# Kernel tuning notes

Measured on AMD Instinct MI355X. Metric: run time of the kernel, lower is better.

The kernel has to match this reference:

```python
import jax, jax.numpy as jnp
import numpy as np

N_TOK = 2048      # flattened batch*seq tokens
D_MODEL = 1024    # in_features
D_INT = 512       # d_intermediate
N_EXPERTS = 8     # n_routed_experts
TOP_K = 2         # n_activated_experts


def setup_inputs() -> dict:
    key = jax.random.key(0)
    k1, k2, k3, k4, k5 = jax.random.split(key, 5)
    x = jax.random.normal(k1, (N_TOK, D_MODEL), dtype=jnp.float32)
    indices = jax.random.randint(k2, (N_TOK, TOP_K), 0, N_EXPERTS, dtype=jnp.int32)
    # router combine weights (normalized over top-k like a softmax router)
    weights = jax.nn.softmax(jax.random.normal(k3, (N_TOK, TOP_K), dtype=jnp.float32), axis=-1)
    # tokens-per-expert counts, consistent with indices (as the router would supply)
    counts = jnp.bincount(indices.reshape(-1), length=N_EXPERTS).astype(jnp.int32)
    # expert weights: fc1 -> 2*d_int (gated MLP), fc2 -> d_model; kaiming-ish scale
    s1 = 1.0 / np.sqrt(D_MODEL)
    s2 = 1.0 / np.sqrt(D_INT)
    fc1_weight = jax.random.uniform(k4, (N_EXPERTS, 2 * D_INT, D_MODEL), jnp.float32, -s1, s1)
    fc2_weight = jax.random.uniform(k5, (N_EXPERTS, D_MODEL, D_INT), jnp.float32, -s2, s2)
    return {"x": x, "weights": weights, "indices": indices, "counts": counts,
            "fc1_weight": fc1_weight, "fc2_weight": fc2_weight}


def reference(x, weights, indices, counts, fc1_weight, fc2_weight):
    # Dense dispatch-free formulation: run every token through every expert's
    # gated MLP, then gather the per-slot expert output. Identical math to the
    # sort / grouped-GEMM / scatter path for the selected (token, expert) pairs.
    # h: (n_tok, n_experts, 2*d_int)
    h = jnp.einsum('td,egd->teg', x, fc1_weight)
    y, z = jnp.split(h, 2, axis=-1)
    a = y * jax.nn.silu(z)  # GatedMLP: y * activation(z)
    # expert outputs: (n_tok, n_experts, d_model)
    out = jnp.einsum('tei,edi->ted', a, fc2_weight)
    # gather the chosen expert output for each of the top-k slots: (n_tok, k, d_model)
    per_slot = jnp.take_along_axis(out, indices[:, :, None], axis=1)
    # combine: z = bmm(weights[:, None], x_by_expert).squeeze(1)
    return jnp.einsum('tk,tkd->td', weights, per_slot)
```

## Files before the change

### kernel.cpp

```cpp
#include <hip/hip_runtime.h>

typedef unsigned short u16;
typedef unsigned int u32;
using short8  = __attribute__((ext_vector_type(8))) short;
using floatx4 = __attribute__((ext_vector_type(4))) float;

#define N_TOK   2048
#define D_MODEL 1024
#define D_INT   512
#define NE      8
#define NPAIR   (N_TOK * 2)
#define ROWS_PAD 5120

#define O_META   0
#define O_ROWOF  4096
#define O_XG     65536
#define O_ACT    10551296
#define O_O2     15794176
#define O_FC1B   36765696
#define O_FC2B   53542912

static __device__ inline u16 f2bf(float f) {
    u32 u = __builtin_bit_cast(u32, f);
    u = (u + 0x7fffu + ((u >> 16) & 1u)) >> 16;
    return (u16)u;
}
static __device__ inline u32 pack2(float a, float b) {
    return (u32)f2bf(a) | ((u32)f2bf(b) << 16);
}

__global__ __launch_bounds__(256) void route_kernel(const int* __restrict__ indices,
                                                    const int* __restrict__ counts,
                                                    int* __restrict__ meta,
                                                    int* __restrict__ row_of) {
    __shared__ int cnt[256][NE];
    __shared__ int off[NE];
    int t = threadIdx.x;
    int idx[16];
    #pragma unroll
    for (int i = 0; i < 16; i++) idx[i] = indices[t * 16 + i];
    int loc[NE];
    #pragma unroll
    for (int e = 0; e < NE; e++) {
        int c = 0;
        #pragma unroll
        for (int i = 0; i < 16; i++) c += (idx[i] == e);
        loc[e] = c;
        cnt[t][e] = c;
    }
    if (t == 0) {
        int acc = 0;
        #pragma unroll
        for (int e = 0; e < NE; e++) {
            off[e] = acc;
            meta[e] = acc;
            acc += ((counts[e] + 127) >> 7) << 7;
        }
        meta[8] = acc;
    }
    __syncthreads();
    for (int d = 1; d < 256; d <<= 1) {
        int v[NE];
        #pragma unroll
        for (int e = 0; e < NE; e++) v[e] = (t >= d) ? cnt[t - d][e] : 0;
        __syncthreads();
        #pragma unroll
        for (int e = 0; e < NE; e++) cnt[t][e] += v[e];
        __syncthreads();
    }
    #pragma unroll
    for (int e = 0; e < NE; e++) cnt[t][e] -= loc[e];
    __syncthreads();
    #pragma unroll
    for (int i = 0; i < 16; i++) {
        int e = idx[i];
        int r = cnt[t][e]++;
        row_of[t * 16 + i] = off[e] + r;
    }
}

__global__ __launch_bounds__(128) void gather_kernel(const float* __restrict__ x,
                                                     const int* __restrict__ row_of,
                                                     u16* __restrict__ Xg) {
    int t = blockIdx.x;
    int tid = threadIdx.x;
    int r0 = row_of[2 * t], r1 = row_of[2 * t + 1];
    const floatx4* src = reinterpret_cast<const floatx4*>(x + (size_t)t * D_MODEL);
    floatx4 a = src[tid * 2];
    floatx4 b = src[tid * 2 + 1];
    uint4 o;
    o.x = pack2(a[0], a[1]); o.y = pack2(a[2], a[3]);
    o.z = pack2(b[0], b[1]); o.w = pack2(b[2], b[3]);
    *reinterpret_cast<uint4*>(Xg + (size_t)r0 * D_MODEL + tid * 8) = o;
    *reinterpret_cast<uint4*>(Xg + (size_t)r1 * D_MODEL + tid * 8) = o;
}

__global__ void convert_w(const float* __restrict__ fc1, const float* __restrict__ fc2,
                          u16* __restrict__ fc1b, u16* __restrict__ fc2b) {
    size_t v = (size_t)blockIdx.x * 256 + threadIdx.x;
    const float* src; u16* dst; size_t off;
    if (v < 1048576) { src = fc1; dst = fc1b; off = v * 8; }
    else             { src = fc2; dst = fc2b; off = (v - 1048576) * 8; }
    const floatx4* s4 = reinterpret_cast<const floatx4*>(src + off);
    floatx4 a = s4[0], b = s4[1];
    uint4 o;
    o.x = pack2(a[0], a[1]); o.y = pack2(a[2], a[3]);
    o.z = pack2(b[0], b[1]); o.w = pack2(b[2], b[3]);
    *reinterpret_cast<uint4*>(dst + off) = o;
}

__global__ __launch_bounds__(256) void gemm1_kernel(
    const u16* __restrict__ Xg, const u16* __restrict__ fc1b,
    u16* __restrict__ Act, const int* __restrict__ meta) {
    __shared__ u16 As[4096];
    __shared__ u16 Bs[4096];
    __shared__ int soff[9];
    int tid = threadIdx.x;
    if (tid < 9) soff[tid] = meta[tid];
    __syncthreads();
    int row0 = blockIdx.y * 128;
    if (row0 >= soff[8]) return;
    int e = 0;
    while (soff[e + 1] <= row0) e++;
    int bx = blockIdx.x;
    const u16* A  = Xg + (size_t)row0 * 1024;
    const u16* Be = fc1b + (size_t)e * 1024 * 1024;

    int lane = tid & 63, w = tid >> 6;
    int m0 = (w >> 1) * 64, n0 = (w & 1) * 32;
    int lr = lane & 15, kq = lane >> 4;

    floatx4 acc[4][4];
    #pragma unroll
    for (int i = 0; i < 4; i++)
        #pragma unroll
        for (int j = 0; j < 4; j++) acc[i][j] = (floatx4){0.f, 0.f, 0.f, 0.f};

    for (int k0 = 0; k0 < 1024; k0 += 32) {
        #pragma unroll
        for (int s = 0; s < 2; s++) {
            int v = tid + s * 256;
            int row = v >> 2, kb = v & 3;
            *reinterpret_cast<uint4*>(&As[(kb * 128 + row) * 8]) =
                *reinterpret_cast<const uint4*>(A + (size_t)row * 1024 + k0 + kb * 8);
            int brow = (row < 64) ? (bx * 64 + row) : (512 + bx * 64 + (row - 64));
            *reinterpret_cast<uint4*>(&Bs[(kb * 128 + row) * 8]) =
                *reinterpret_cast<const uint4*>(Be + (size_t)brow * 1024 + k0 + kb * 8);
        }
        __syncthreads();
        short8 af[4], bf[4];
        #pragma unroll
        for (int i = 0; i < 4; i++)
            af[i] = *reinterpret_cast<const short8*>(&As[(kq * 128 + m0 + i * 16 + lr) * 8]);
        #pragma unroll
        for (int j = 0; j < 4; j++) {
            int nn = (j < 2) ? (n0 + j * 16) : (64 + n0 + (j - 2) * 16);
            bf[j] = *reinterpret_cast<const short8*>(&Bs[(kq * 128 + nn + lr) * 8]);
        }
        #pragma unroll
        for (int i = 0; i < 4; i++)
            #pragma unroll
            for (int j = 0; j < 4; j++)
                acc[i][j] = __builtin_amdgcn_mfma_f32_16x16x32_bf16(af[i], bf[j], acc[i][j], 0, 0, 0);
        __syncthreads();
    }
    #pragma unroll
    for (int i = 0; i < 4; i++) {
        #pragma unroll
        for (int jy = 0; jy < 2; jy++) {
            floatx4 y = acc[i][jy], z = acc[i][jy + 2];
            #pragma unroll
            for (int r = 0; r < 4; r++) {
                float zz = z[r];
                float av = y[r] * (zz / (1.0f + __expf(-zz)));
                int m = m0 + i * 16 + kq * 4 + r;
                int g = bx * 64 + n0 + jy * 16 + lr;
                Act[(size_t)(row0 + m) * D_INT + g] = f2bf(av);
            }
        }
    }
}

__global__ __launch_bounds__(256) void gemm2_kernel(
    const u16* __restrict__ Act, const u16* __restrict__ fc2b,
    float* __restrict__ O2, const int* __restrict__ meta) {
    __shared__ u16 As[4096];
    __shared__ u16 Bs[4096];
    __shared__ int soff[9];
    int tid = threadIdx.x;
    if (tid < 9) soff[tid] = meta[tid];
    __syncthreads();
    int row0 = blockIdx.y * 128;
    if (row0 >= soff[8]) return;
    int e = 0;
    while (soff[e + 1] <= row0) e++;
    int bx = blockIdx.x;
    const u16* A  = Act + (size_t)row0 * 512;
    const u16* Be = fc2b + (size_t)e * 1024 * 512;

    int lane = tid & 63, w = tid >> 6;
    int m0 = (w >> 1) * 64, n0 = (w & 1) * 64;
    int lr = lane & 15, kq = lane >> 4;

    floatx4 acc[4][4];
    #pragma unroll
    for (int i = 0; i < 4; i++)
        #pragma unroll
        for (int j = 0; j < 4; j++) acc[i][j] = (floatx4){0.f, 0.f, 0.f, 0.f};

    for (int k0 = 0; k0 < 512; k0 += 32) {
        #pragma unroll
        for (int s = 0; s < 2; s++) {
            int v = tid + s * 256;
            int row = v >> 2, kb = v & 3;
            *reinterpret_cast<uint4*>(&As[(kb * 128 + row) * 8]) =
                *reinterpret_cast<const uint4*>(A + (size_t)row * 512 + k0 + kb * 8);
            *reinterpret_cast<uint4*>(&Bs[(kb * 128 + row) * 8]) =
                *reinterpret_cast<const uint4*>(Be + (size_t)(bx * 128 + row) * 512 + k0 + kb * 8);
        }
        __syncthreads();
        short8 af[4], bf[4];
        #pragma unroll
        for (int i = 0; i < 4; i++)
            af[i] = *reinterpret_cast<const short8*>(&As[(kq * 128 + m0 + i * 16 + lr) * 8]);
        #pragma unroll
        for (int j = 0; j < 4; j++)
            bf[j] = *reinterpret_cast<const short8*>(&Bs[(kq * 128 + n0 + j * 16 + lr) * 8]);
        #pragma unroll
        for (int i = 0; i < 4; i++)
            #pragma unroll
            for (int j = 0; j < 4; j++)
                acc[i][j] = __builtin_amdgcn_mfma_f32_16x16x32_bf16(af[i], bf[j], acc[i][j], 0, 0, 0);
        __syncthreads();
    }
    #pragma unroll
    for (int i = 0; i < 4; i++)
        #pragma unroll
        for (int j = 0; j < 4; j++) {
            #pragma unroll
            for (int r = 0; r < 4; r++) {
                int m = m0 + i * 16 + kq * 4 + r;
                int n = bx * 128 + n0 + j * 16 + lr;
                O2[(size_t)(row0 + m) * D_MODEL + n] = acc[i][j][r];
            }
        }
}

__global__ void combine_kernel(const float* __restrict__ O2,
                               const float* __restrict__ wts,
                               const int* __restrict__ row_of,
                               float* __restrict__ out) {
    int t = blockIdx.x;
    int tid = threadIdx.x;
    int r0 = row_of[2 * t], r1 = row_of[2 * t + 1];
    float w0 = wts[2 * t], w1 = wts[2 * t + 1];
    const floatx4* p0 = reinterpret_cast<const floatx4*>(O2 + (size_t)r0 * D_MODEL);
    const floatx4* p1 = reinterpret_cast<const floatx4*>(O2 + (size_t)r1 * D_MODEL);
    floatx4 v = w0 * p0[tid] + w1 * p1[tid];
    reinterpret_cast<floatx4*>(out + (size_t)t * D_MODEL)[tid] = v;
}

extern "C" void kernel_launch(void* const* d_in, const int* in_sizes, int n_in,
                              void* d_out, int out_size, void* d_ws, size_t ws_size,
                              hipStream_t stream) {
    const float* x       = (const float*)d_in[0];
    const float* wts     = (const float*)d_in[1];
    const int*   indices = (const int*)d_in[2];
    const int*   counts  = (const int*)d_in[3];
    const float* fc1     = (const float*)d_in[4];
    const float* fc2     = (const float*)d_in[5];
    float* out = (float*)d_out;
    char* ws = (char*)d_ws;

    int*  meta   = (int*)(ws + O_META);
    int*  row_of = (int*)(ws + O_ROWOF);
    u16*  Xg     = (u16*)(ws + O_XG);
    u16*  Act    = (u16*)(ws + O_ACT);
    float* O2    = (float*)(ws + O_O2);
    u16*  fc1b   = (u16*)(ws + O_FC1B);
    u16*  fc2b   = (u16*)(ws + O_FC2B);

    route_kernel<<<1, 256, 0, stream>>>(indices, counts, meta, row_of);
    convert_w<<<6144, 256, 0, stream>>>(fc1, fc2, fc1b, fc2b);
    gather_kernel<<<N_TOK, 128, 0, stream>>>(x, row_of, Xg);
    gemm1_kernel<<<dim3(8, 40), 256, 0, stream>>>(Xg, fc1b, Act, meta);
    gemm2_kernel<<<dim3(8, 40), 256, 0, stream>>>(Act, fc2b, O2, meta);
    combine_kernel<<<N_TOK, 256, 0, stream>>>(O2, wts, row_of, out);
}
```

Before: 167.5 us.

## Fuse combine into gemm2 via atomics and use direct global-to-LDS loads with swizzle

The separate combine kernel and the fp32 O2 intermediate are removed. gemm2 now scales each row by its router weight and atomically adds it into a zero-initialised output, using a pair_of map built in the route kernel. Both GEMMs now load tiles with global_load_lds straight into an XOR-swizzled row-major LDS layout, which removes the register staging and is meant to reduce bank conflicts. The cost is a memset and fp32 atomic traffic, and the sum order becomes nondeterministic.

```diff
diff --git a/kernel.cpp b/kernel.cpp
--- a/kernel.cpp
+++ b/kernel.cpp
@@ -9,14 +9,13 @@
 #define D_MODEL 1024
 #define D_INT   512
 #define NE      8
-#define NPAIR   (N_TOK * 2)
 #define ROWS_PAD 5120
 
 #define O_META   0
 #define O_ROWOF  4096
+#define O_PAIR   20480
 #define O_XG     65536
 #define O_ACT    10551296
-#define O_O2     15794176
 #define O_FC1B   36765696
 #define O_FC2B   53542912
 
@@ -28,14 +27,22 @@
 static __device__ inline u32 pack2(float a, float b) {
     return (u32)f2bf(a) | ((u32)f2bf(b) << 16);
 }
+static __device__ inline void glds16(const u16* g, u16* l) {
+    __builtin_amdgcn_global_load_lds(
+        (const __attribute__((address_space(1))) void*)g,
+        (__attribute__((address_space(3))) void*)l, 16, 0, 0);
+}
 
 __global__ __launch_bounds__(256) void route_kernel(const int* __restrict__ indices,
                                                     const int* __restrict__ counts,
                                                     int* __restrict__ meta,
-                                                    int* __restrict__ row_of) {
+                                                    int* __restrict__ row_of,
+                                                    int* __restrict__ pair_of) {
     __shared__ int cnt[256][NE];
     __shared__ int off[NE];
     int t = threadIdx.x;
+    #pragma unroll
+    for (int i = 0; i < 20; i++) pair_of[t * 20 + i] = -1;
     int idx[16];
     #pragma unroll
     for (int i = 0; i < 16; i++) idx[i] = indices[t * 16 + i];
@@ -75,7 +82,9 @@
     for (int i = 0; i < 16; i++) {
         int e = idx[i];
         int r = cnt[t][e]++;
-        row_of[t * 16 + i] = off[e] + r;
+        int row = off[e] + r;
+        row_of[t * 16 + i] = row;
+        pair_of[row] = t * 16 + i;
     }
 }
 
@@ -129,6 +138,21 @@
     int lane = tid & 63, w = tid >> 6;
     int m0 = (w >> 1) * 64, n0 = (w & 1) * 32;
     int lr = lane & 15, kq = lane >> 4;
+    int ka = ((kq ^ ((lr >> 1) & 3)) * 8);
+
+    int v0 = tid, v1 = tid + 256;
+    int r0s = v0 >> 2, kb0 = (v0 & 3) ^ ((r0s >> 1) & 3);
+    int r1s = v1 >> 2, kb1 = (v1 & 3) ^ ((r1s >> 1) & 3);
+    int brow0 = (r0s < 64) ? bx * 64 + r0s : 448 + bx * 64 + r0s;
+    int brow1 = (r1s < 64) ? bx * 64 + r1s : 448 + bx * 64 + r1s;
+    u16* lA0 = As + (w * 64) * 8;
+    u16* lA1 = As + (w * 64 + 256) * 8;
+    u16* lB0 = Bs + (w * 64) * 8;
+    u16* lB1 = Bs + (w * 64 + 256) * 8;
+    const u16* gA0 = A + (size_t)r0s * 1024 + kb0 * 8;
+    const u16* gA1 = A + (size_t)r1s * 1024 + kb1 * 8;
+    const u16* gB0 = Be + (size_t)brow0 * 1024 + kb0 * 8;
+    const u16* gB1 = Be + (size_t)brow1 * 1024 + kb1 * 8;
 
     floatx4 acc[4][4];
     #pragma unroll
@@ -137,25 +161,19 @@
         for (int j = 0; j < 4; j++) acc[i][j] = (floatx4){0.f, 0.f, 0.f, 0.f};
 
     for (int k0 = 0; k0 < 1024; k0 += 32) {
-        #pragma unroll
-        for (int s = 0; s < 2; s++) {
-            int v = tid + s * 256;
-            int row = v >> 2, kb = v & 3;
-            *reinterpret_cast<uint4*>(&As[(kb * 128 + row) * 8]) =
-                *reinterpret_cast<const uint4*>(A + (size_t)row * 1024 + k0 + kb * 8);
-            int brow = (row < 64) ? (bx * 64 + row) : (512 + bx * 64 + (row - 64));
-            *reinterpret_cast<uint4*>(&Bs[(kb * 128 + row) * 8]) =
-                *reinterpret_cast<const uint4*>(Be + (size_t)brow * 1024 + k0 + kb * 8);
-        }
+        glds16(gA0 + k0, lA0);
+        glds16(gA1 + k0, lA1);
+        glds16(gB0 + k0, lB0);
+        glds16(gB1 + k0, lB1);
         __syncthreads();
         short8 af[4], bf[4];
         #pragma unroll
         for (int i = 0; i < 4; i++)
-            af[i] = *reinterpret_cast<const short8*>(&As[(kq * 128 + m0 + i * 16 + lr) * 8]);
+            af[i] = *reinterpret_cast<const short8*>(&As[(m0 + i * 16 + lr) * 32 + ka]);
         #pragma unroll
         for (int j = 0; j < 4; j++) {
             int nn = (j < 2) ? (n0 + j * 16) : (64 + n0 + (j - 2) * 16);
-            bf[j] = *reinterpret_cast<const short8*>(&Bs[(kq * 128 + nn + lr) * 8]);
+            bf[j] = *reinterpret_cast<const short8*>(&Bs[(nn + lr) * 32 + ka]);
         }
         #pragma unroll
         for (int i = 0; i < 4; i++)
@@ -183,10 +201,13 @@
 
 __global__ __launch_bounds__(256) void gemm2_kernel(
     const u16* __restrict__ Act, const u16* __restrict__ fc2b,
-    float* __restrict__ O2, const int* __restrict__ meta) {
+    float* __restrict__ out, const int* __restrict__ meta,
+    const int* __restrict__ pair_of, const float* __restrict__ wts) {
     __shared__ u16 As[4096];
     __shared__ u16 Bs[4096];
     __shared__ int soff[9];
+    __shared__ int sPair[128];
+    __shared__ float sW[128];
     int tid = threadIdx.x;
     if (tid < 9) soff[tid] = meta[tid];
     __syncthreads();
@@ -201,6 +222,19 @@
     int lane = tid & 63, w = tid >> 6;
     int m0 = (w >> 1) * 64, n0 = (w & 1) * 64;
     int lr = lane & 15, kq = lane >> 4;
+    int ka = ((kq ^ ((lr >> 1) & 3)) * 8);
+
+    int v0 = tid, v1 = tid + 256;
+    int r0s = v0 >> 2, kb0 = (v0 & 3) ^ ((r0s >> 1) & 3);
+    int r1s = v1 >> 2, kb1 = (v1 & 3) ^ ((r1s >> 1) & 3);
+    u16* lA0 = As + (w * 64) * 8;
+    u16* lA1 = As + (w * 64 + 256) * 8;
+    u16* lB0 = Bs + (w * 64) * 8;
+    u16* lB1 = Bs + (w * 64 + 256) * 8;
+    const u16* gA0 = A + (size_t)r0s * 512 + kb0 * 8;
+    const u16* gA1 = A + (size_t)r1s * 512 + kb1 * 8;
+    const u16* gB0 = Be + (size_t)(bx * 128 + r0s) * 512 + kb0 * 8;
+    const u16* gB1 = Be + (size_t)(bx * 128 + r1s) * 512 + kb1 * 8;
 
     floatx4 acc[4][4];
     #pragma unroll
@@ -209,23 +243,18 @@
         for (int j = 0; j < 4; j++) acc[i][j] = (floatx4){0.f, 0.f, 0.f, 0.f};
 
     for (int k0 = 0; k0 < 512; k0 += 32) {
-        #pragma unroll
-        for (int s = 0; s < 2; s++) {
-            int v = tid + s * 256;
-            int row = v >> 2, kb = v & 3;
-            *reinterpret_cast<uint4*>(&As[(kb * 128 + row) * 8]) =
-                *reinterpret_cast<const uint4*>(A + (size_t)row * 512 + k0 + kb * 8);
-            *reinterpret_cast<uint4*>(&Bs[(kb * 128 + row) * 8]) =
-                *reinterpret_cast<const uint4*>(Be + (size_t)(bx * 128 + row) * 512 + k0 + kb * 8);
-        }
+        glds16(gA0 + k0, lA0);
+        glds16(gA1 + k0, lA1);
+        glds16(gB0 + k0, lB0);
+        glds16(gB1 + k0, lB1);
         __syncthreads();
         short8 af[4], bf[4];
         #pragma unroll
         for (int i = 0; i < 4; i++)
-            af[i] = *reinterpret_cast<const short8*>(&As[(kq * 128 + m0 + i * 16 + lr) * 8]);
+            af[i] = *reinterpret_cast<const short8*>(&As[(m0 + i * 16 + lr) * 32 + ka]);
         #pragma unroll
         for (int j = 0; j < 4; j++)
-            bf[j] = *reinterpret_cast<const short8*>(&Bs[(kq * 128 + n0 + j * 16 + lr) * 8]);
+            bf[j] = *reinterpret_cast<const short8*>(&Bs[(n0 + j * 16 + lr) * 32 + ka]);
         #pragma unroll
         for (int i = 0; i < 4; i++)
             #pragma unroll
@@ -233,31 +262,26 @@
                 acc[i][j] = __builtin_amdgcn_mfma_f32_16x16x32_bf16(af[i], bf[j], acc[i][j], 0, 0, 0);
         __syncthreads();
     }
+    if (tid < 128) {
+        int p = pair_of[row0 + tid];
+        sPair[tid] = p;
+        sW[tid] = (p >= 0) ? wts[p] : 0.f;
+    }
+    __syncthreads();
     #pragma unroll
     for (int i = 0; i < 4; i++)
         #pragma unroll
-        for (int j = 0; j < 4; j++) {
-            #pragma unroll
-            for (int r = 0; r < 4; r++) {
-                int m = m0 + i * 16 + kq * 4 + r;
-                int n = bx * 128 + n0 + j * 16 + lr;
-                O2[(size_t)(row0 + m) * D_MODEL + n] = acc[i][j][r];
+        for (int r = 0; r < 4; r++) {
+            int m = m0 + i * 16 + kq * 4 + r;
+            int p = sPair[m];
+            if (p >= 0) {
+                float wgt = sW[m];
+                float* dst = out + (size_t)(p >> 1) * D_MODEL + bx * 128;
+                #pragma unroll
+                for (int j = 0; j < 4; j++)
+                    atomicAdd(dst + n0 + j * 16 + lr, wgt * acc[i][j][r]);
             }
         }
-}
-
-__global__ void combine_kernel(const float* __restrict__ O2,
-                               const float* __restrict__ wts,
-                               const int* __restrict__ row_of,
-                               float* __restrict__ out) {
-    int t = blockIdx.x;
-    int tid = threadIdx.x;
-    int r0 = row_of[2 * t], r1 = row_of[2 * t + 1];
-    float w0 = wts[2 * t], w1 = wts[2 * t + 1];
-    const floatx4* p0 = reinterpret_cast<const floatx4*>(O2 + (size_t)r0 * D_MODEL);
-    const floatx4* p1 = reinterpret_cast<const floatx4*>(O2 + (size_t)r1 * D_MODEL);
-    floatx4 v = w0 * p0[tid] + w1 * p1[tid];
-    reinterpret_cast<floatx4*>(out + (size_t)t * D_MODEL)[tid] = v;
 }
 
 extern "C" void kernel_launch(void* const* d_in, const int* in_sizes, int n_in,
@@ -272,18 +296,18 @@
     float* out = (float*)d_out;
     char* ws = (char*)d_ws;
 
-    int*  meta   = (int*)(ws + O_META);
-    int*  row_of = (int*)(ws + O_ROWOF);
-    u16*  Xg     = (u16*)(ws + O_XG);
-    u16*  Act    = (u16*)(ws + O_ACT);
-    float* O2    = (float*)(ws + O_O2);
-    u16*  fc1b   = (u16*)(ws + O_FC1B);
-    u16*  fc2b   = (u16*)(ws + O_FC2B);
-
-    route_kernel<<<1, 256, 0, stream>>>(indices, counts, meta, row_of);
+    int*  meta    = (int*)(ws + O_META);
+    int*  row_of  = (int*)(ws + O_ROWOF);
+    int*  pair_of = (int*)(ws + O_PAIR);
+    u16*  Xg      = (u16*)(ws + O_XG);
+    u16*  Act     = (u16*)(ws + O_ACT);
+    u16*  fc1b    = (u16*)(ws + O_FC1B);
+    u16*  fc2b    = (u16*)(ws + O_FC2B);
+
+    hipMemsetAsync(d_out, 0, (size_t)out_size * sizeof(float), stream);
+    route_kernel<<<1, 256, 0, stream>>>(indices, counts, meta, row_of, pair_of);
     convert_w<<<6144, 256, 0, stream>>>(fc1, fc2, fc1b, fc2b);
     gather_kernel<<<N_TOK, 128, 0, stream>>>(x, row_of, Xg);
     gemm1_kernel<<<dim3(8, 40), 256, 0, stream>>>(Xg, fc1b, Act, meta);
-    gemm2_kernel<<<dim3(8, 40), 256, 0, stream>>>(Act, fc2b, O2, meta);
-    combine_kernel<<<N_TOK, 256, 0, stream>>>(O2, wts, row_of, out);
-}
+    gemm2_kernel<<<dim3(8, 40), 256, 0, stream>>>(Act, fc2b, out, meta, pair_of, wts);
+}
```

Result: faster. 163.6 us (-2.4%).
